# Performance work log

Hardware: AMD Instinct MI355X
Metric: run time of the kernel (lower is better)

Reference implementation:

```python
import jax, jax.numpy as jnp
import numpy as np

NUM_HEADS = 8
TOPK_RATIO = 0.1


def setup_inputs() -> dict:
    key = jax.random.key(0)
    ks = jax.random.split(key, 5)
    B, N, C = 1, 8192, 512
    S = 16              # num_frames
    K = 4               # clusters
    x = jax.random.normal(ks[0], (B, N, C), dtype=jnp.float32)
    w_qkv = jax.random.normal(ks[1], (3 * C, C), dtype=jnp.float32) * (C ** -0.5)
    b_qkv = jax.random.normal(ks[2], (3 * C,), dtype=jnp.float32) * 0.02
    w_proj = jax.random.normal(ks[3], (C, C), dtype=jnp.float32) * (C ** -0.5)
    b_proj = jax.random.normal(ks[4], (C,), dtype=jnp.float32) * 0.02
    keyframes = jnp.arange(K, dtype=jnp.int64 if jax.config.jax_enable_x64 else jnp.int32) * (S // K)  # [0,4,8,12]
    clusters = jnp.arange(S, dtype=keyframes.dtype).reshape(K, S // K)  # 4 clusters of 4 frames
    return {"x": x, "w_qkv": w_qkv, "b_qkv": b_qkv, "w_proj": w_proj,
            "b_proj": b_proj, "keyframes": keyframes, "clusters": clusters,
            "num_frames": S}


def _hierarchy_attn(q, k, v, keyframes, clusters, num_frames):
    # q,k,v: [B,H,N,D]
    B, H, N, D = q.shape
    scale = D ** -0.5
    tpf = N // num_frames                     # tokens per frame
    K = clusters.shape[0]
    tok = jnp.arange(tpf)
    # keyframe query token indices: [K*tpf]
    key_q_idx = (keyframes[:, None] * tpf + tok[None, :]).reshape(-1)
    q_proto = q[:, :, key_q_idx, :]           # [B,H,K*tpf,D]
    # proto attention scores vs all keys: [B,H,K*tpf,N]
    scores = jnp.einsum('bhqd,bhnd->bhqn', q_proto * scale, k)
    # aggregate per cluster (over batch, heads, keyframe tokens) -> [K,N]
    agg = scores.reshape(B, H, K, tpf, N).mean(axis=(0, 1, 3))
    topk_num = max(1, int(tpf * K * TOPK_RATIO))
    _, topk_idx = jax.lax.top_k(agg, topk_num)          # [K, T]
    # cluster query token indices: [K, M] with M = frames_per_cluster*tpf
    cluster_q_idx = (clusters[:, :, None] * tpf + tok[None, None, :]).reshape(K, -1)
    q_c = q[:, :, cluster_q_idx, :]           # [B,H,K,M,D]
    k_c = k[:, :, topk_idx, :]                # [B,H,K,T,D]
    v_c = v[:, :, topk_idx, :]                # [B,H,K,T,D]
    attn = jax.nn.softmax(jnp.einsum('bhkmd,bhktd->bhkmt', q_c * scale, k_c), axis=-1)
    x_c = jnp.einsum('bhkmt,bhktd->bhkmd', attn, v_c)   # [B,H,K,M,D]
    x_out = jnp.zeros_like(q)
    x_out = x_out.at[:, :, cluster_q_idx.reshape(-1), :].set(
        x_c.reshape(B, H, K * x_c.shape[3], D))
    return x_out


def reference(x, w_qkv, b_qkv, w_proj, b_proj, keyframes, clusters, num_frames):
    B, N, C = x.shape
    H = NUM_HEADS
    D = C // H
    qkv = (x @ w_qkv.T + b_qkv).reshape(B, N, 3, H, D)
    qkv = jnp.transpose(qkv, (2, 0, 3, 1, 4))           # [3,B,H,N,D]
    q, k, v = qkv[0], qkv[1], qkv[2]
    x_out = _hierarchy_attn(q, k, v, keyframes, clusters, num_frames)  # [B,H,N,D]
    x_out = jnp.transpose(x_out, (0, 2, 1, 3)).reshape(B, N, C)
    return x_out @ w_proj.T + b_proj
```

## Files before the change

### kernel.cpp

```cpp
#include <hip/hip_runtime.h>
#include <hip/hip_bf16.h>

#define N_TOK 8192
#define C_DIM 512
#define NH 8
#define DH 64
#define KCLUST 4
#define TPF 512
#define TOPK 204
#define KVPAD 256
#define MPC 2048

#define WS_WQH    0
#define WS_WPH    393216
#define WS_QHI    524288
#define WS_KC     2621440
#define WS_VC     2883584
#define WS_XAHI   3145728
#define WS_XBARP  5242880
#define WS_QBAR   5275648
#define WS_G      5277696
#define WS_AGG    5279744

using frag16 = __attribute__((ext_vector_type(8))) short;
using f32x4  = __attribute__((ext_vector_type(4))) float;

__device__ __forceinline__ unsigned short f2bf(float x) {
  unsigned u = __float_as_uint(x);
  return (unsigned short)((u + 0x7fffu + ((u >> 16) & 1u)) >> 16);
}
__device__ __forceinline__ float bf2f(unsigned short h) {
  return __uint_as_float(((unsigned)h) << 16);
}
__device__ __forceinline__ unsigned pkbf(float a, float b) {
  __hip_bfloat162 t = __float22bfloat162_rn(make_float2(a, b));
  return *reinterpret_cast<unsigned*>(&t);
}

__global__ __launch_bounds__(256) void prep_xbar(
    const float* __restrict__ x, const int* __restrict__ keyframes,
    float* __restrict__ xbarp) {
  const int b = blockIdx.x, tid = threadIdx.x;
  int kk = b >> 4, s = b & 15;
  int base = keyframes[kk] * TPF + s * 32;
  float a0 = 0.f, a1 = 0.f;
  for (int t = 0; t < 32; t++) {
    a0 += x[(size_t)(base + t) * C_DIM + tid];
    a1 += x[(size_t)(base + t) * C_DIM + tid + 256];
  }
  xbarp[(kk * 16 + s) * C_DIM + tid] = a0;
  xbarp[(kk * 16 + s) * C_DIM + tid + 256] = a1;
}

__global__ __launch_bounds__(256) void qbar_wide(
    const float* __restrict__ w_qkv, const float* __restrict__ b_qkv,
    const float* __restrict__ xbarp, float* __restrict__ qbar) {
  __shared__ float xs[C_DIM];
  const int b = blockIdx.x, tid = threadIdx.x;
  const int kk = b & 3, h = (b >> 2) & 7, dg = b >> 5;
  for (int i = tid; i < C_DIM; i += 256) {
    float a = 0.f;
    for (int s = 0; s < 16; s++) a += xbarp[(kk * 16 + s) * C_DIM + i];
    xs[i] = a * (1.f / 512.f);
  }
  __syncthreads();
  const int wave = tid >> 6, lane = tid & 63;
  const int og = wave * 2 + (lane >> 5), lt = lane & 31;
  const int d = dg * 8 + og;
  const float4* w4 =
      reinterpret_cast<const float4*>(w_qkv + (size_t)(h * 64 + d) * C_DIM + lt * 16);
  const float4* x4 = reinterpret_cast<const float4*>(&xs[lt * 16]);
  float a = 0.f;
#pragma unroll
  for (int q = 0; q < 4; q++) {
    float4 wv = w4[q], xv = x4[q];
    a += wv.x * xv.x + wv.y * xv.y + wv.z * xv.z + wv.w * xv.w;
  }
#pragma unroll
  for (int off = 16; off >= 1; off >>= 1) a += __shfl_xor(a, off);
  if (lt == 0) qbar[(h * 4 + kk) * 64 + d] = a + b_qkv[h * 64 + d];
}

__global__ __launch_bounds__(256) void g_wide(
    const float* __restrict__ w_qkv, const float* __restrict__ qbar,
    float* __restrict__ g) {
  __shared__ float qs[C_DIM];
  __shared__ float red[16][16];
  const int b = blockIdx.x, tid = threadIdx.x;
  const int kk = b >> 5, cs = b & 31;
  for (int i = tid; i < C_DIM; i += 256)
    qs[i] = qbar[((i >> 6) * 4 + kk) * 64 + (i & 63)];
  __syncthreads();
  const int jg = tid >> 4, cl = tid & 15;
  const int c = cs * 16 + cl;
  const float* wk = w_qkv + (size_t)C_DIM * C_DIM + c;
  float a = 0.f;
#pragma unroll 4
  for (int j = jg * 32; j < jg * 32 + 32; j++)
    a += qs[j] * wk[(size_t)j * C_DIM];
  red[jg][cl] = a;
  __syncthreads();
  if (tid < 16) {
    float s = red[0][tid];
#pragma unroll
    for (int q = 1; q < 16; q++) s += red[q][tid];
    g[kk * C_DIM + cs * 16 + tid] = s;
  }
}

__global__ __launch_bounds__(256) void agg_wcvt(
    const float* __restrict__ x, const float* __restrict__ g,
    float* __restrict__ agg, const float* __restrict__ w_qkv,
    const float* __restrict__ w_proj, unsigned short* __restrict__ wqh,
    unsigned short* __restrict__ wph) {
  __shared__ float gs[KCLUST][C_DIM];
  const int bid = blockIdx.x, tid = threadIdx.x;
  if (bid >= 2048) {
    int bx = bid - 2048;
    const float* src = (bx < 768) ? w_qkv : w_proj;
    unsigned short* dst = (bx < 768) ? wqh : wph;
    int i = ((bx < 768) ? bx : (bx - 768)) * 256 + tid;
    float4 v = reinterpret_cast<const float4*>(src)[i];
    reinterpret_cast<uint2*>(dst)[i] = make_uint2(pkbf(v.x, v.y), pkbf(v.z, v.w));
    return;
  }
  for (int i = tid; i < KCLUST * C_DIM; i += 256) gs[i >> 9][i & 511] = g[i];
  __syncthreads();
  int wave = tid >> 6, lane = tid & 63;
  int n = bid * 4 + wave;
  const float4* xp = reinterpret_cast<const float4*>(x + (size_t)n * C_DIM);
  float4 xa = xp[lane], xb = xp[lane + 64];
  float a[4];
#pragma unroll
  for (int kk = 0; kk < 4; kk++) {
    const float4* gpv = reinterpret_cast<const float4*>(&gs[kk][0]);
    float4 ga = gpv[lane], gb2 = gpv[lane + 64];
    a[kk] = xa.x * ga.x + xa.y * ga.y + xa.z * ga.z + xa.w * ga.w +
            xb.x * gb2.x + xb.y * gb2.y + xb.z * gb2.z + xb.w * gb2.w;
  }
#pragma unroll
  for (int off = 32; off >= 1; off >>= 1) {
    a[0] += __shfl_xor(a[0], off);
    a[1] += __shfl_xor(a[1], off);
    a[2] += __shfl_xor(a[2], off);
    a[3] += __shfl_xor(a[3], off);
  }
  if (lane == 0) {
    agg[0 * N_TOK + n] = a[0];
    agg[1 * N_TOK + n] = a[1];
    agg[2 * N_TOK + n] = a[2];
    agg[3 * N_TOK + n] = a[3];
  }
}

__device__ __forceinline__ int block_scan_incl(int v, int* wsum, int tid) {
  int lane = tid & 63, wv = tid >> 6;
#pragma unroll
  for (int off = 1; off < 64; off <<= 1) {
    int t = __shfl_up(v, off, 64);
    if (lane >= off) v += t;
  }
  if (lane == 63) wsum[wv] = v;
  __syncthreads();
  if (wv > 0) v += wsum[0];
  if (wv > 1) v += wsum[1];
  if (wv > 2) v += wsum[2];
  __syncthreads();
  return v;
}

#define APAN 1032
#define BUFS 8256
__global__ __launch_bounds__(256) void gemm_qkv2(
    const float* __restrict__ x, const unsigned short* __restrict__ Bhi,
    const float* __restrict__ bias, const float* __restrict__ agg,
    unsigned short* __restrict__ qhi, unsigned short* __restrict__ kc,
    unsigned short* __restrict__ vc) {
  __shared__ __align__(16) short pool[17828];
  const int tid = threadIdx.x;
  const int bid = blockIdx.x;
  const int wave = tid >> 6, lane = tid & 63;
  const int qd = lane >> 4, ln = lane & 15;

  if (bid < 512) {
    const int grp = bid >> 5;
    const int rem = bid & 31;
    const int j0 = (rem >> 3) * 128;
    const int m0 = (grp * 8 + (rem & 7)) * 64;
    const int rh = wave >> 1, ch = wave & 1;

    short* As = pool;
    short* Bs = pool + 4096;

    const int arow = tid & 63, ap = tid >> 6;
    const int brow = tid & 127, bp = tid >> 7;
    const float4* pA4 =
        reinterpret_cast<const float4*>(x + (size_t)(m0 + arow) * C_DIM) + ap * 2;
    const unsigned short* pB0 = Bhi + (size_t)(j0 + brow) * C_DIM + bp * 8;
    const unsigned short* pB1 = pB0 + 16;

    f32x4 acc[2][4] = {};

    float4 fa0 = pA4[0], fa1 = pA4[1];
    uint4 rb0 = *reinterpret_cast<const uint4*>(pB0);
    uint4 rb1 = *reinterpret_cast<const uint4*>(pB1);
    *reinterpret_cast<uint4*>(&As[ap * 512 + arow * 8]) =
        make_uint4(pkbf(fa0.x, fa0.y), pkbf(fa0.z, fa0.w),
                   pkbf(fa1.x, fa1.y), pkbf(fa1.z, fa1.w));
    *reinterpret_cast<uint4*>(&Bs[bp * 1024 + brow * 8]) = rb0;
    *reinterpret_cast<uint4*>(&Bs[(bp + 2) * 1024 + brow * 8]) = rb1;
    __syncthreads();

    int cur = 0;
#pragma unroll
    for (int it = 0; it < 16; it++) {
      if (it < 15) {
        int k4 = (it + 1) * 8;
        fa0 = pA4[k4];
        fa1 = pA4[k4 + 1];
        rb0 = *reinterpret_cast<const uint4*>(pB0 + (it + 1) * 32);
        rb1 = *reinterpret_cast<const uint4*>(pB1 + (it + 1) * 32);
      }
      frag16 a_h[2], b_h[4];
#pragma unroll
      for (int i = 0; i < 2; i++)
        a_h[i] = *reinterpret_cast<const frag16*>(
            &As[cur * 2048 + qd * 512 + (rh * 32 + i * 16 + ln) * 8]);
#pragma unroll
      for (int j = 0; j < 4; j++)
        b_h[j] = *reinterpret_cast<const frag16*>(
            &Bs[cur * 4096 + qd * 1024 + (ch * 64 + j * 16 + ln) * 8]);
#pragma unroll
      for (int i = 0; i < 2; i++)
#pragma unroll
        for (int j = 0; j < 4; j++)
          acc[i][j] = __builtin_amdgcn_mfma_f32_16x16x32_bf16(a_h[i], b_h[j], acc[i][j], 0, 0, 0);
      if (it < 15) {
        int nxt = cur ^ 1;
        *reinterpret_cast<uint4*>(&As[nxt * 2048 + ap * 512 + arow * 8]) =
            make_uint4(pkbf(fa0.x, fa0.y), pkbf(fa0.z, fa0.w),
                       pkbf(fa1.x, fa1.y), pkbf(fa1.z, fa1.w));
        *reinterpret_cast<uint4*>(&Bs[nxt * 4096 + bp * 1024 + brow * 8]) = rb0;
        *reinterpret_cast<uint4*>(&Bs[nxt * 4096 + (bp + 2) * 1024 + brow * 8]) = rb1;
        __syncthreads();
        cur = nxt;
      }
    }

    __syncthreads();
    short* sh = pool;
#pragma unroll
    for (int i = 0; i < 2; i++)
#pragma unroll
      for (int j = 0; j < 4; j++) {
        int jcol = ch * 64 + j * 16 + ln;
        float bv = bias[j0 + jcol];
#pragma unroll
        for (int r = 0; r < 4; r++) {
          int mrow = rh * 32 + i * 16 + qd * 4 + r;
          sh[mrow * 136 + jcol] = (short)f2bf((acc[i][j][r] + bv) * 0.125f);
        }
      }
    __syncthreads();
#pragma unroll
    for (int p = 0; p < 4; p++) {
      int u = tid + p * 256;
      int row = u >> 4, c = (u & 15) * 8;
      int hh = ((j0 + c) >> 6) & 7, d0 = c & 63;
      *reinterpret_cast<uint4*>(qhi + ((size_t)hh * N_TOK + m0 + row) * DH + d0) =
          *reinterpret_cast<const uint4*>(&sh[row * 136 + c]);
    }
    return;
  }

  const int b2 = bid - 512;
  const int kk = b2 >> 4;
  const int sub = b2 & 15;
  const int mloc = (sub >> 3) * 128;
  const int j0 = 512 + (sub & 7) * 128;
  const int wr = wave >> 1, wc = wave & 1;

  const int r0 = tid >> 2, p0 = tid & 3;
  const int r1 = r0 + 64;
  const float4 *pA0, *pA1;
  {
    unsigned* sk = reinterpret_cast<unsigned*>(pool);
    int* hist = reinterpret_cast<int*>(pool + 16384);
    int* scn = reinterpret_cast<int*>(pool + 16896);
    int* wsum = reinterpret_cast<int*>(pool + 17408);
    int* selv = reinterpret_cast<int*>(pool + 17416);
    int* idxl = reinterpret_cast<int*>(pool + 17420);
    const float* row = agg + (size_t)kk * N_TOK;

    for (int i = tid; i < N_TOK; i += 256) {
      unsigned u = __float_as_uint(row[i]);
      sk[i] = (u & 0x80000000u) ? ~u : (u | 0x80000000u);
    }
    __syncthreads();

    unsigned prefix = 0;
    int remaining = TOPK;
#pragma unroll
    for (int rnd = 3; rnd >= 0; rnd--) {
      int shift = rnd * 8;
      hist[tid] = 0;
      __syncthreads();
      for (int i = tid; i < N_TOK; i += 256) {
        unsigned key = sk[i];
        bool in = (rnd == 3) || ((key >> (shift + 8)) == prefix);
        if (in) atomicAdd(&hist[(key >> shift) & 255], 1);
      }
      __syncthreads();
      int sv = block_scan_incl(hist[255 - tid], wsum, tid);
      scn[tid] = sv;
      __syncthreads();
      int b = tid;
      int cgt = (b == 255) ? 0 : scn[254 - b];
      if (cgt < remaining && remaining <= cgt + hist[b]) {
        selv[0] = b;
        selv[1] = remaining - cgt;
      }
      __syncthreads();
      prefix = (prefix << 8) | (unsigned)selv[0];
      remaining = selv[1];
      __syncthreads();
    }
    unsigned kth = prefix;
    int base = tid * 32;

    int cA = 0;
    for (int i = 0; i < 32; i++) cA += (sk[base + i] > kth) ? 1 : 0;
    int sA = block_scan_incl(cA, wsum, tid);
    scn[tid] = sA;
    __syncthreads();
    int exclA = sA - cA;
    int G = scn[255];
    int p = exclA;
    for (int i = 0; i < 32; i++)
      if (sk[base + i] > kth) idxl[p++] = base + i;
    __syncthreads();

    int cB = 0;
    for (int i = 0; i < 32; i++) cB += (sk[base + i] == kth) ? 1 : 0;
    int sB = block_scan_incl(cB, wsum, tid);
    int exclB = sB - cB;
    int pos = G + exclB;
    for (int i = 0; i < 32; i++) {
      if (sk[base + i] == kth) {
        if (pos < TOPK) idxl[pos] = base + i;
        pos++;
      }
    }
    __syncthreads();

    int t0i = mloc + r0, t1i = mloc + r1;
    if (t0i > TOPK - 1) t0i = TOPK - 1;
    if (t1i > TOPK - 1) t1i = TOPK - 1;
    const int tok0 = idxl[t0i];
    const int tok1 = idxl[t1i];
    __syncthreads();

    pA0 = reinterpret_cast<const float4*>(x + (size_t)tok0 * C_DIM) + p0 * 2;
    pA1 = reinterpret_cast<const float4*>(x + (size_t)tok1 * C_DIM) + p0 * 2;
  }
  const unsigned short* pB0 = Bhi + (size_t)(j0 + r0) * C_DIM + p0 * 8;
  const unsigned short* pB1 = Bhi + (size_t)(j0 + r1) * C_DIM + p0 * 8;

  f32x4 acc[4][4] = {};

  float4 fa[4];
  uint4 rb[2];
  fa[0] = pA0[0]; fa[1] = pA0[1];
  fa[2] = pA1[0]; fa[3] = pA1[1];
  rb[0] = *reinterpret_cast<const uint4*>(pB0);
  rb[1] = *reinterpret_cast<const uint4*>(pB1);

  {
    *reinterpret_cast<uint4*>(&pool[p0 * APAN + r0 * 8]) =
        make_uint4(pkbf(fa[0].x, fa[0].y), pkbf(fa[0].z, fa[0].w),
                   pkbf(fa[1].x, fa[1].y), pkbf(fa[1].z, fa[1].w));
    *reinterpret_cast<uint4*>(&pool[p0 * APAN + r1 * 8]) =
        make_uint4(pkbf(fa[2].x, fa[2].y), pkbf(fa[2].z, fa[2].w),
                   pkbf(fa[3].x, fa[3].y), pkbf(fa[3].z, fa[3].w));
    *reinterpret_cast<uint4*>(&pool[4 * APAN + p0 * APAN + r0 * 8]) = rb[0];
    *reinterpret_cast<uint4*>(&pool[4 * APAN + p0 * APAN + r1 * 8]) = rb[1];
  }
  __syncthreads();

  int cur = 0;
#pragma unroll
  for (int it = 0; it < 16; it++) {
    if (it < 15) {
      int k4 = (it + 1) * 8;
      fa[0] = pA0[k4]; fa[1] = pA0[k4 + 1];
      fa[2] = pA1[k4]; fa[3] = pA1[k4 + 1];
      rb[0] = *reinterpret_cast<const uint4*>(pB0 + (it + 1) * 32);
      rb[1] = *reinterpret_cast<const uint4*>(pB1 + (it + 1) * 32);
    }
    const int bb = cur * BUFS;
    frag16 a_h[4], b_h[4];
#pragma unroll
    for (int i = 0; i < 4; i++) {
      int row = wr * 64 + i * 16 + ln;
      a_h[i] = *reinterpret_cast<const frag16*>(&pool[bb + qd * APAN + row * 8]);
    }
#pragma unroll
    for (int j = 0; j < 4; j++) {
      int row = wc * 64 + j * 16 + ln;
      b_h[j] = *reinterpret_cast<const frag16*>(&pool[bb + 4 * APAN + qd * APAN + row * 8]);
    }
#pragma unroll
    for (int i = 0; i < 4; i++)
#pragma unroll
      for (int j = 0; j < 4; j++)
        acc[i][j] = __builtin_amdgcn_mfma_f32_16x16x32_bf16(a_h[i], b_h[j], acc[i][j], 0, 0, 0);

    if (it < 15) {
      const int nb = (cur ^ 1) * BUFS;
      *reinterpret_cast<uint4*>(&pool[nb + p0 * APAN + r0 * 8]) =
          make_uint4(pkbf(fa[0].x, fa[0].y), pkbf(fa[0].z, fa[0].w),
                     pkbf(fa[1].x, fa[1].y), pkbf(fa[1].z, fa[1].w));
      *reinterpret_cast<uint4*>(&pool[nb + p0 * APAN + r1 * 8]) =
          make_uint4(pkbf(fa[2].x, fa[2].y), pkbf(fa[2].z, fa[2].w),
                     pkbf(fa[3].x, fa[3].y), pkbf(fa[3].z, fa[3].w));
      *reinterpret_cast<uint4*>(&pool[nb + 4 * APAN + p0 * APAN + r0 * 8]) = rb[0];
      *reinterpret_cast<uint4*>(&pool[nb + 4 * APAN + p0 * APAN + r1 * 8]) = rb[1];
    }
    __syncthreads();
    cur ^= 1;
  }

  const int sel = j0 >> 9;
  short* sh = pool;
#pragma unroll
  for (int i = 0; i < 4; i++)
#pragma unroll
    for (int j = 0; j < 4; j++) {
      int jcol = wc * 64 + j * 16 + ln;
      float bv = bias[j0 + jcol];
#pragma unroll
      for (int r = 0; r < 4; r++) {
        int mrow = wr * 64 + i * 16 + qd * 4 + r;
        sh[mrow * 136 + jcol] = (short)f2bf(acc[i][j][r] + bv);
      }
    }
  __syncthreads();
  unsigned short* dstc = (sel == 1) ? kc : vc;
#pragma unroll
  for (int p = 0; p < 8; p++) {
    int u = tid + p * 256;
    int row = u >> 4, c = (u & 15) * 8;
    int hh = ((j0 + c) >> 6) & 7, d0 = c & 63;
    *reinterpret_cast<uint4*>(
        dstc + (((size_t)kk * 8 + hh) * KVPAD + mloc + row) * DH + d0) =
        *reinterpret_cast<const uint4*>(&sh[row * 136 + c]);
  }
}

__global__ __launch_bounds__(256) void flash_mfma(
    const unsigned short* __restrict__ qhi, const unsigned short* __restrict__ kc,
    const unsigned short* __restrict__ vc, const int* __restrict__ clusters,
    unsigned short* __restrict__ xahi) {
  __shared__ short Ks[64 * 72];
  __shared__ short Vs[64 * 72];
  __shared__ short Ps[128 * 72];
  const int tid = threadIdx.x;
  const int qb = blockIdx.x, kk = blockIdx.y, h = blockIdx.z;
  const int wave = tid >> 6, lane = tid & 63;
  const int ln = lane & 15, qd = lane >> 4;

  const int q_local0 = qb * 128;
  const int frame = clusters[kk * 4 + (q_local0 >> 9)];
  const int tokbase = frame * TPF + (q_local0 & 511);
  const size_t kvbase = ((size_t)kk * 8 + h) * KVPAD * DH;

  frag16 qa_h[2][2];
#pragma unroll
  for (int mt = 0; mt < 2; mt++) {
    const int tok_m = tokbase + wave * 32 + mt * 16 + ln;
    const unsigned short* qr_h = qhi + ((size_t)h * N_TOK + tok_m) * DH;
#pragma unroll
    for (int s = 0; s < 2; s++)
      qa_h[mt][s] = *reinterpret_cast<const frag16*>(qr_h + s * 32 + qd * 8);
  }

  f32x4 acc_o[2][4] = {};
  float lsum[2][4] = {};

  for (int t0 = 0; t0 < 192; t0 += 64) {
#pragma unroll
    for (int i = 0; i < 2; i++) {
      int u = tid + i * 256;
      int r = u >> 3, oct = u & 7;
      *reinterpret_cast<frag16*>(&Ks[r * 72 + oct * 8]) =
          *reinterpret_cast<const frag16*>(kc + kvbase + (size_t)(t0 + r) * DH + oct * 8);
    }
    {
      int tk = (tid & 15) * 4, td = (tid >> 4) * 4;
      uint2 w2[4];
#pragma unroll
      for (int i = 0; i < 4; i++)
        w2[i] = *reinterpret_cast<const uint2*>(vc + kvbase + (size_t)(t0 + tk + i) * DH + td);
#pragma unroll
      for (int dd = 0; dd < 4; dd++) {
        unsigned s0 = (dd < 2) ? (w2[0].x >> (16 * dd)) : (w2[0].y >> (16 * (dd - 2)));
        unsigned s1 = (dd < 2) ? (w2[1].x >> (16 * dd)) : (w2[1].y >> (16 * (dd - 2)));
        unsigned s2 = (dd < 2) ? (w2[2].x >> (16 * dd)) : (w2[2].y >> (16 * (dd - 2)));
        unsigned s3 = (dd < 2) ? (w2[3].x >> (16 * dd)) : (w2[3].y >> (16 * (dd - 2)));
        *reinterpret_cast<uint2*>(&Vs[(td + dd) * 72 + tk]) =
            make_uint2((s0 & 0xffffu) | (s1 << 16), (s2 & 0xffffu) | (s3 << 16));
      }
    }
    __syncthreads();

#pragma unroll
    for (int mt = 0; mt < 2; mt++) {
      f32x4 sacc[4] = {};
#pragma unroll
      for (int c = 0; c < 4; c++) {
#pragma unroll
        for (int s = 0; s < 2; s++) {
          frag16 bh = *reinterpret_cast<const frag16*>(&Ks[(c * 16 + ln) * 72 + s * 32 + qd * 8]);
          sacc[c] = __builtin_amdgcn_mfma_f32_16x16x32_bf16(qa_h[mt][s], bh, sacc[c], 0, 0, 0);
        }
      }
#pragma unroll
      for (int c = 0; c < 4; c++) {
#pragma unroll
        for (int r = 0; r < 4; r++) {
          float p = __expf(sacc[c][r]);
          lsum[mt][r] += p;
          Ps[(wave * 32 + mt * 16 + qd * 4 + r) * 72 + c * 16 + ln] = (short)f2bf(p);
        }
      }
    }

#pragma unroll
    for (int mt = 0; mt < 2; mt++)
#pragma unroll
      for (int s = 0; s < 2; s++) {
        frag16 pa = *reinterpret_cast<const frag16*>(
            &Ps[(wave * 32 + mt * 16 + ln) * 72 + s * 32 + qd * 8]);
#pragma unroll
        for (int dt = 0; dt < 4; dt++) {
          frag16 vb = *reinterpret_cast<const frag16*>(&Vs[(dt * 16 + ln) * 72 + s * 32 + qd * 8]);
          acc_o[mt][dt] = __builtin_amdgcn_mfma_f32_16x16x32_bf16(pa, vb, acc_o[mt][dt], 0, 0, 0);
        }
      }
    __syncthreads();
  }

  {
    const int t0 = 192;
#pragma unroll
    for (int i = 0; i < 2; i++) {
      int u = tid + i * 256;
      int r = u >> 3, oct = u & 7;
      *reinterpret_cast<frag16*>(&Ks[r * 72 + oct * 8]) =
          *reinterpret_cast<const frag16*>(kc + kvbase + (size_t)(t0 + r) * DH + oct * 8);
    }
    {
      int tk = (tid & 15) * 4, td = (tid >> 4) * 4;
      uint2 w2[4];
#pragma unroll
      for (int i = 0; i < 4; i++)
        w2[i] = *reinterpret_cast<const uint2*>(vc + kvbase + (size_t)(t0 + tk + i) * DH + td);
#pragma unroll
      for (int dd = 0; dd < 4; dd++) {
        unsigned s0 = (dd < 2) ? (w2[0].x >> (16 * dd)) : (w2[0].y >> (16 * (dd - 2)));
        unsigned s1 = (dd < 2) ? (w2[1].x >> (16 * dd)) : (w2[1].y >> (16 * (dd - 2)));
        unsigned s2 = (dd < 2) ? (w2[2].x >> (16 * dd)) : (w2[2].y >> (16 * (dd - 2)));
        unsigned s3 = (dd < 2) ? (w2[3].x >> (16 * dd)) : (w2[3].y >> (16 * (dd - 2)));
        *reinterpret_cast<uint2*>(&Vs[(td + dd) * 72 + tk]) =
            make_uint2((s0 & 0xffffu) | (s1 << 16), (s2 & 0xffffu) | (s3 << 16));
      }
    }
    __syncthreads();

#pragma unroll
    for (int mt = 0; mt < 2; mt++) {
      f32x4 sacc = {};
#pragma unroll
      for (int s = 0; s < 2; s++) {
        frag16 bh = *reinterpret_cast<const frag16*>(&Ks[ln * 72 + s * 32 + qd * 8]);
        sacc = __builtin_amdgcn_mfma_f32_16x16x32_bf16(qa_h[mt][s], bh, sacc, 0, 0, 0);
      }
#pragma unroll
      for (int r = 0; r < 4; r++) {
        float p = (ln < 12) ? __expf(sacc[r]) : 0.f;
        lsum[mt][r] += p;
        int prow = (wave * 32 + mt * 16 + qd * 4 + r) * 72;
        Ps[prow + ln] = (short)f2bf(p);
        Ps[prow + 16 + ln] = 0;
      }
    }

#pragma unroll
    for (int mt = 0; mt < 2; mt++) {
      frag16 pa = *reinterpret_cast<const frag16*>(
          &Ps[(wave * 32 + mt * 16 + ln) * 72 + qd * 8]);
#pragma unroll
      for (int dt = 0; dt < 4; dt++) {
        frag16 vb = *reinterpret_cast<const frag16*>(&Vs[(dt * 16 + ln) * 72 + qd * 8]);
        acc_o[mt][dt] = __builtin_amdgcn_mfma_f32_16x16x32_bf16(pa, vb, acc_o[mt][dt], 0, 0, 0);
      }
    }
  }

#pragma unroll
  for (int mt = 0; mt < 2; mt++)
#pragma unroll
    for (int r = 0; r < 4; r++) {
      float l = lsum[mt][r];
      l += __shfl_xor(l, 1);
      l += __shfl_xor(l, 2);
      l += __shfl_xor(l, 4);
      l += __shfl_xor(l, 8);
      lsum[mt][r] = 1.f / l;
    }

#pragma unroll
  for (int mt = 0; mt < 2; mt++)
#pragma unroll
    for (int dt = 0; dt < 4; dt++)
#pragma unroll
      for (int r = 0; r < 4; r++)
        Ps[(wave * 32 + mt * 16 + qd * 4 + r) * 72 + dt * 16 + ln] =
            (short)f2bf(acc_o[mt][dt][r] * lsum[mt][r]);
  __syncthreads();
#pragma unroll
  for (int p = 0; p < 4; p++) {
    int u = tid + p * 256;
    int row = u >> 3, c = (u & 7) * 8;
    *reinterpret_cast<uint4*>(xahi + (size_t)(tokbase + row) * C_DIM + h * DH + c) =
        *reinterpret_cast<const uint4*>(&Ps[row * 72 + c]);
  }
}

__global__ __launch_bounds__(256) void gemm_proj(
    const unsigned short* __restrict__ Ahi, const unsigned short* __restrict__ Bhi,
    const float* __restrict__ bias, float* __restrict__ out) {
  __shared__ short pool[12288];
  short* As = pool;
  short* Bs = pool + 4096;
  const int tid = threadIdx.x;
  const int bid = blockIdx.x;
  const int grp = bid / 32;
  const int rem = bid - grp * 32;
  const int jblk = rem >> 3;
  const int m_idx = grp * 8 + (rem & 7);
  const int j0 = jblk * 128;
  const int m0 = m_idx * 64;
  const int wave = tid >> 6, lane = tid & 63;
  const int rh = wave >> 1, ch = wave & 1;
  const int qd = lane >> 4, ln = lane & 15;

  const int arow = tid & 63, ap = tid >> 6;
  const int brow = tid & 127, bp = tid >> 7;
  const unsigned short* pA = Ahi + (size_t)(m0 + arow) * C_DIM + ap * 8;
  const unsigned short* pB0 = Bhi + (size_t)(j0 + brow) * C_DIM + bp * 8;
  const unsigned short* pB1 = pB0 + 16;

  f32x4 acc[2][4] = {};

  uint4 ra = *reinterpret_cast<const uint4*>(pA);
  uint4 rb0 = *reinterpret_cast<const uint4*>(pB0);
  uint4 rb1 = *reinterpret_cast<const uint4*>(pB1);
  *reinterpret_cast<uint4*>(&As[ap * 512 + arow * 8]) = ra;
  *reinterpret_cast<uint4*>(&Bs[bp * 1024 + brow * 8]) = rb0;
  *reinterpret_cast<uint4*>(&Bs[(bp + 2) * 1024 + brow * 8]) = rb1;
  __syncthreads();

  int cur = 0;
#pragma unroll
  for (int it = 0; it < 16; it++) {
    if (it < 15) {
      int k = (it + 1) * 32;
      ra = *reinterpret_cast<const uint4*>(pA + k);
      rb0 = *reinterpret_cast<const uint4*>(pB0 + k);
      rb1 = *reinterpret_cast<const uint4*>(pB1 + k);
    }
    frag16 a_h[2], b_h[4];
#pragma unroll
    for (int i = 0; i < 2; i++)
      a_h[i] = *reinterpret_cast<const frag16*>(&As[cur * 2048 + qd * 512 + (rh * 32 + i * 16 + ln) * 8]);
#pragma unroll
    for (int j = 0; j < 4; j++)
      b_h[j] = *reinterpret_cast<const frag16*>(&Bs[cur * 4096 + qd * 1024 + (ch * 64 + j * 16 + ln) * 8]);
#pragma unroll
    for (int i = 0; i < 2; i++)
#pragma unroll
      for (int j = 0; j < 4; j++)
        acc[i][j] = __builtin_amdgcn_mfma_f32_16x16x32_bf16(a_h[i], b_h[j], acc[i][j], 0, 0, 0);
    if (it < 15) {
      int nxt = cur ^ 1;
      *reinterpret_cast<uint4*>(&As[nxt * 2048 + ap * 512 + arow * 8]) = ra;
      *reinterpret_cast<uint4*>(&Bs[nxt * 4096 + bp * 1024 + brow * 8]) = rb0;
      *reinterpret_cast<uint4*>(&Bs[nxt * 4096 + (bp + 2) * 1024 + brow * 8]) = rb1;
      __syncthreads();
      cur = nxt;
    }
  }

  float* sh32 = reinterpret_cast<float*>(pool);
#pragma unroll
  for (int chp = 0; chp < 2; chp++) {
    __syncthreads();
    if (ch == chp) {
#pragma unroll
      for (int i = 0; i < 2; i++)
#pragma unroll
        for (int j = 0; j < 4; j++) {
          int jcol = j * 16 + ln;
          float bv = bias[j0 + chp * 64 + jcol];
#pragma unroll
          for (int r = 0; r < 4; r++)
            sh32[(rh * 32 + i * 16 + qd * 4 + r) * 68 + jcol] = acc[i][j][r] + bv;
        }
    }
    __syncthreads();
#pragma unroll
    for (int p = 0; p < 4; p++) {
      int u = tid + p * 256;
      int row = u >> 4, c4 = (u & 15) * 4;
      *reinterpret_cast<float4*>(out + (size_t)(m0 + row) * C_DIM + j0 + chp * 64 + c4) =
          *reinterpret_cast<const float4*>(&sh32[row * 68 + c4]);
    }
  }
}

extern "C" void kernel_launch(void* const* d_in, const int* in_sizes, int n_in,
                              void* d_out, int out_size, void* d_ws, size_t ws_size,
                              hipStream_t stream) {
  const float* x = (const float*)d_in[0];
  const float* w_qkv = (const float*)d_in[1];
  const float* b_qkv = (const float*)d_in[2];
  const float* w_proj = (const float*)d_in[3];
  const float* b_proj = (const float*)d_in[4];
  const int* keyframes = (const int*)d_in[5];
  const int* clusters = (const int*)d_in[6];
  float* out = (float*)d_out;
  float* ws = (float*)d_ws;

  unsigned short* wqh = (unsigned short*)(ws + WS_WQH);
  unsigned short* wph = (unsigned short*)(ws + WS_WPH);
  unsigned short* qhi = (unsigned short*)(ws + WS_QHI);
  unsigned short* kc = (unsigned short*)(ws + WS_KC);
  unsigned short* vc = (unsigned short*)(ws + WS_VC);
  unsigned short* xahi = (unsigned short*)(ws + WS_XAHI);
  float* xbarp = ws + WS_XBARP;
  float* qbar = ws + WS_QBAR;
  float* g = ws + WS_G;
  float* agg = ws + WS_AGG;

  prep_xbar<<<64, 256, 0, stream>>>(x, keyframes, xbarp);
  qbar_wide<<<256, 256, 0, stream>>>(w_qkv, b_qkv, xbarp, qbar);
  g_wide<<<128, 256, 0, stream>>>(w_qkv, qbar, g);
  agg_wcvt<<<3072, 256, 0, stream>>>(x, g, agg, w_qkv, w_proj, wqh, wph);
  gemm_qkv2<<<576, 256, 0, stream>>>(x, wqh, b_qkv, agg, qhi, kc, vc);
  flash_mfma<<<dim3(MPC / 128, KCLUST, NH), 256, 0, stream>>>(
      qhi, kc, vc, clusters, xahi);
  gemm_proj<<<512, 256, 0, stream>>>(xahi, wph, b_proj, out);
}
```

Before: 174.8 us.

## Pre-tile x and w_qkv into bf16 LDS-ready panels for QKV GEMM

The conversion kernel now writes w_qkv as bf16 in a pre-tiled panel layout matching the GEMM's shared-memory staging. It also writes a bf16 pre-tiled copy of x for the Q-projection blocks. The QKV GEMM then streams contiguous uint4 chunks straight into LDS, with no fp32 loads, packing or strided row addressing in its main loop. In exchange, the extra x conversion pass adds global traffic and another workspace buffer before the GEMM.

Measured after the change: 183.3 us. +4.9%, slower.

```diff
diff --git a/kernel.cpp b/kernel.cpp
--- a/kernel.cpp
+++ b/kernel.cpp
@@ -11,7 +11,7 @@
 #define KVPAD 256
 #define MPC 2048
 
-#define WS_WQH    0
+#define WS_WQKVT  0
 #define WS_WPH    393216
 #define WS_QHI    524288
 #define WS_KC     2621440
@@ -21,6 +21,7 @@
 #define WS_QBAR   5275648
 #define WS_G      5277696
 #define WS_AGG    5279744
+#define WS_XT     6291456
 
 using frag16 = __attribute__((ext_vector_type(8))) short;
 using f32x4  = __attribute__((ext_vector_type(4))) float;
@@ -108,20 +109,56 @@
   }
 }
 
-__global__ __launch_bounds__(256) void agg_wcvt(
+__global__ __launch_bounds__(256) void agg_cvt(
     const float* __restrict__ x, const float* __restrict__ g,
     float* __restrict__ agg, const float* __restrict__ w_qkv,
-    const float* __restrict__ w_proj, unsigned short* __restrict__ wqh,
-    unsigned short* __restrict__ wph) {
+    const float* __restrict__ w_proj, unsigned short* __restrict__ wqkvt,
+    unsigned short* __restrict__ wph, unsigned short* __restrict__ xt) {
   __shared__ float gs[KCLUST][C_DIM];
   const int bid = blockIdx.x, tid = threadIdx.x;
+  if (bid >= 2496) {
+    int b0 = (bid - 2496) * 4;
+#pragma unroll
+    for (int q = 0; q < 4; q++) {
+      int ts = b0 + q;
+      int mt = ts >> 4, sl = ts & 15;
+      int row = tid & 63, ap = tid >> 6;
+      const float4* src = reinterpret_cast<const float4*>(
+          x + (size_t)(mt * 64 + row) * C_DIM + sl * 32 + ap * 8);
+      float4 v0 = src[0], v1 = src[1];
+      *reinterpret_cast<uint4*>(xt + (size_t)ts * 2048 + tid * 8) =
+          make_uint4(pkbf(v0.x, v0.y), pkbf(v0.z, v0.w),
+                     pkbf(v1.x, v1.y), pkbf(v1.z, v1.w));
+    }
+    return;
+  }
+  if (bid >= 2240) {
+    int i = (bid - 2240) * 256 + tid;
+    float4 v = reinterpret_cast<const float4*>(w_proj)[i];
+    reinterpret_cast<uint2*>(wph)[i] = make_uint2(pkbf(v.x, v.y), pkbf(v.z, v.w));
+    return;
+  }
   if (bid >= 2048) {
-    int bx = bid - 2048;
-    const float* src = (bx < 768) ? w_qkv : w_proj;
-    unsigned short* dst = (bx < 768) ? wqh : wph;
-    int i = ((bx < 768) ? bx : (bx - 768)) * 256 + tid;
-    float4 v = reinterpret_cast<const float4*>(src)[i];
-    reinterpret_cast<uint2*>(dst)[i] = make_uint2(pkbf(v.x, v.y), pkbf(v.z, v.w));
+    int b = bid - 2048;
+    int jt = b >> 4, sl = b & 15;
+    {
+      int p = tid >> 7, row = tid & 127;
+      const float4* src = reinterpret_cast<const float4*>(
+          w_qkv + (size_t)(jt * 128 + row) * C_DIM + sl * 32 + p * 8);
+      float4 v0 = src[0], v1 = src[1];
+      *reinterpret_cast<uint4*>(wqkvt + (size_t)(jt * 16 + sl) * 4096 + tid * 8) =
+          make_uint4(pkbf(v0.x, v0.y), pkbf(v0.z, v0.w),
+                     pkbf(v1.x, v1.y), pkbf(v1.z, v1.w));
+    }
+    {
+      int p = 2 + (tid >> 7), row = tid & 127;
+      const float4* src = reinterpret_cast<const float4*>(
+          w_qkv + (size_t)(jt * 128 + row) * C_DIM + sl * 32 + p * 8);
+      float4 v0 = src[0], v1 = src[1];
+      *reinterpret_cast<uint4*>(wqkvt + (size_t)(jt * 16 + sl) * 4096 + 2048 + tid * 8) =
+          make_uint4(pkbf(v0.x, v0.y), pkbf(v0.z, v0.w),
+                     pkbf(v1.x, v1.y), pkbf(v1.z, v1.w));
+    }
     return;
   }
   for (int i = tid; i < KCLUST * C_DIM; i += 256) gs[i >> 9][i & 511] = g[i];
@@ -172,10 +209,10 @@
 #define APAN 1032
 #define BUFS 8256
 __global__ __launch_bounds__(256) void gemm_qkv2(
-    const float* __restrict__ x, const unsigned short* __restrict__ Bhi,
-    const float* __restrict__ bias, const float* __restrict__ agg,
-    unsigned short* __restrict__ qhi, unsigned short* __restrict__ kc,
-    unsigned short* __restrict__ vc) {
+    const float* __restrict__ x, const unsigned short* __restrict__ wqkvt,
+    const unsigned short* __restrict__ xt, const float* __restrict__ bias,
+    const float* __restrict__ agg, unsigned short* __restrict__ qhi,
+    unsigned short* __restrict__ kc, unsigned short* __restrict__ vc) {
   __shared__ __align__(16) short pool[17828];
   const int tid = threadIdx.x;
   const int bid = blockIdx.x;
@@ -185,41 +222,35 @@
   if (bid < 512) {
     const int grp = bid >> 5;
     const int rem = bid & 31;
-    const int j0 = (rem >> 3) * 128;
+    const int jt = rem >> 3;
+    const int j0 = jt * 128;
     const int m0 = (grp * 8 + (rem & 7)) * 64;
+    const int mt = m0 >> 6;
     const int rh = wave >> 1, ch = wave & 1;
 
     short* As = pool;
     short* Bs = pool + 4096;
 
-    const int arow = tid & 63, ap = tid >> 6;
-    const int brow = tid & 127, bp = tid >> 7;
-    const float4* pA4 =
-        reinterpret_cast<const float4*>(x + (size_t)(m0 + arow) * C_DIM) + ap * 2;
-    const unsigned short* pB0 = Bhi + (size_t)(j0 + brow) * C_DIM + bp * 8;
-    const unsigned short* pB1 = pB0 + 16;
+    const unsigned short* pA = xt + (size_t)(mt * 16) * 2048 + tid * 8;
+    const unsigned short* pB = wqkvt + (size_t)(jt * 16) * 4096 + tid * 8;
 
     f32x4 acc[2][4] = {};
 
-    float4 fa0 = pA4[0], fa1 = pA4[1];
-    uint4 rb0 = *reinterpret_cast<const uint4*>(pB0);
-    uint4 rb1 = *reinterpret_cast<const uint4*>(pB1);
-    *reinterpret_cast<uint4*>(&As[ap * 512 + arow * 8]) =
-        make_uint4(pkbf(fa0.x, fa0.y), pkbf(fa0.z, fa0.w),
-                   pkbf(fa1.x, fa1.y), pkbf(fa1.z, fa1.w));
-    *reinterpret_cast<uint4*>(&Bs[bp * 1024 + brow * 8]) = rb0;
-    *reinterpret_cast<uint4*>(&Bs[(bp + 2) * 1024 + brow * 8]) = rb1;
+    uint4 ra = *reinterpret_cast<const uint4*>(pA);
+    uint4 rb0 = *reinterpret_cast<const uint4*>(pB);
+    uint4 rb1 = *reinterpret_cast<const uint4*>(pB + 2048);
+    *reinterpret_cast<uint4*>(&As[tid * 8]) = ra;
+    *reinterpret_cast<uint4*>(&Bs[tid * 8]) = rb0;
+    *reinterpret_cast<uint4*>(&Bs[2048 + tid * 8]) = rb1;
     __syncthreads();
 
     int cur = 0;
 #pragma unroll
     for (int it = 0; it < 16; it++) {
       if (it < 15) {
-        int k4 = (it + 1) * 8;
-        fa0 = pA4[k4];
-        fa1 = pA4[k4 + 1];
-        rb0 = *reinterpret_cast<const uint4*>(pB0 + (it + 1) * 32);
-        rb1 = *reinterpret_cast<const uint4*>(pB1 + (it + 1) * 32);
+        ra = *reinterpret_cast<const uint4*>(pA + (it + 1) * 2048);
+        rb0 = *reinterpret_cast<const uint4*>(pB + (it + 1) * 4096);
+        rb1 = *reinterpret_cast<const uint4*>(pB + (it + 1) * 4096 + 2048);
       }
       frag16 a_h[2], b_h[4];
 #pragma unroll
@@ -237,11 +268,9 @@
           acc[i][j] = __builtin_amdgcn_mfma_f32_16x16x32_bf16(a_h[i], b_h[j], acc[i][j], 0, 0, 0);
       if (it < 15) {
         int nxt = cur ^ 1;
-        *reinterpret_cast<uint4*>(&As[nxt * 2048 + ap * 512 + arow * 8]) =
-            make_uint4(pkbf(fa0.x, fa0.y), pkbf(fa0.z, fa0.w),
-                       pkbf(fa1.x, fa1.y), pkbf(fa1.z, fa1.w));
-        *reinterpret_cast<uint4*>(&Bs[nxt * 4096 + bp * 1024 + brow * 8]) = rb0;
-        *reinterpret_cast<uint4*>(&Bs[nxt * 4096 + (bp + 2) * 1024 + brow * 8]) = rb1;
+        *reinterpret_cast<uint4*>(&As[nxt * 2048 + tid * 8]) = ra;
+        *reinterpret_cast<uint4*>(&Bs[nxt * 4096 + tid * 8]) = rb0;
+        *reinterpret_cast<uint4*>(&Bs[nxt * 4096 + 2048 + tid * 8]) = rb1;
         __syncthreads();
         cur = nxt;
       }
@@ -277,7 +306,8 @@
   const int kk = b2 >> 4;
   const int sub = b2 & 15;
   const int mloc = (sub >> 3) * 128;
-  const int j0 = 512 + (sub & 7) * 128;
+  const int jt = 4 + (sub & 7);
+  const int j0 = jt * 128;
   const int wr = wave >> 1, wc = wave & 1;
 
   const int r0 = tid >> 2, p0 = tid & 3;
@@ -363,8 +393,7 @@
     pA0 = reinterpret_cast<const float4*>(x + (size_t)tok0 * C_DIM) + p0 * 2;
     pA1 = reinterpret_cast<const float4*>(x + (size_t)tok1 * C_DIM) + p0 * 2;
   }
-  const unsigned short* pB0 = Bhi + (size_t)(j0 + r0) * C_DIM + p0 * 8;
-  const unsigned short* pB1 = Bhi + (size_t)(j0 + r1) * C_DIM + p0 * 8;
+  const unsigned short* pBt = wqkvt + (size_t)(jt * 16) * 4096;
 
   f32x4 acc[4][4] = {};
 
@@ -372,8 +401,8 @@
   uint4 rb[2];
   fa[0] = pA0[0]; fa[1] = pA0[1];
   fa[2] = pA1[0]; fa[3] = pA1[1];
-  rb[0] = *reinterpret_cast<const uint4*>(pB0);
-  rb[1] = *reinterpret_cast<const uint4*>(pB1);
+  rb[0] = *reinterpret_cast<const uint4*>(pBt + p0 * 1024 + r0 * 8);
+  rb[1] = *reinterpret_cast<const uint4*>(pBt + p0 * 1024 + r1 * 8);
 
   {
     *reinterpret_cast<uint4*>(&pool[p0 * APAN + r0 * 8]) =
@@ -394,8 +423,8 @@
       int k4 = (it + 1) * 8;
       fa[0] = pA0[k4]; fa[1] = pA0[k4 + 1];
       fa[2] = pA1[k4]; fa[3] = pA1[k4 + 1];
-      rb[0] = *reinterpret_cast<const uint4*>(pB0 + (it + 1) * 32);
-      rb[1] = *reinterpret_cast<const uint4*>(pB1 + (it + 1) * 32);
+      rb[0] = *reinterpret_cast<const uint4*>(pBt + (it + 1) * 4096 + p0 * 1024 + r0 * 8);
+      rb[1] = *reinterpret_cast<const uint4*>(pBt + (it + 1) * 4096 + p0 * 1024 + r1 * 8);
     }
     const int bb = cur * BUFS;
     frag16 a_h[4], b_h[4];
@@ -742,12 +771,13 @@
   float* out = (float*)d_out;
   float* ws = (float*)d_ws;
 
-  unsigned short* wqh = (unsigned short*)(ws + WS_WQH);
+  unsigned short* wqkvt = (unsigned short*)(ws + WS_WQKVT);
   unsigned short* wph = (unsigned short*)(ws + WS_WPH);
   unsigned short* qhi = (unsigned short*)(ws + WS_QHI);
   unsigned short* kc = (unsigned short*)(ws + WS_KC);
   unsigned short* vc = (unsigned short*)(ws + WS_VC);
   unsigned short* xahi = (unsigned short*)(ws + WS_XAHI);
+  unsigned short* xt = (unsigned short*)(ws + WS_XT);
   float* xbarp = ws + WS_XBARP;
   float* qbar = ws + WS_QBAR;
   float* g = ws + WS_G;
@@ -756,8 +786,8 @@
   prep_xbar<<<64, 256, 0, stream>>>(x, keyframes, xbarp);
   qbar_wide<<<256, 256, 0, stream>>>(w_qkv, b_qkv, xbarp, qbar);
   g_wide<<<128, 256, 0, stream>>>(w_qkv, qbar, g);
-  agg_wcvt<<<3072, 256, 0, stream>>>(x, g, agg, w_qkv, w_proj, wqh, wph);
-  gemm_qkv2<<<576, 256, 0, stream>>>(x, wqh, b_qkv, agg, qhi, kc, vc);
+  agg_cvt<<<3008, 256, 0, stream>>>(x, g, agg, w_qkv, w_proj, wqkvt, wph, xt);
+  gemm_qkv2<<<576, 256, 0, stream>>>(x, wqkvt, xt, b_qkv, agg, qhi, kc, vc);
   flash_mfma<<<dim3(MPC / 128, KCLUST, NH), 256, 0, stream>>>(
       qhi, kc, vc, clusters, xahi);
   gemm_proj<<<512, 256, 0, stream>>>(xahi, wph, b_proj, out);
```
